# Optimization experiments

Hardware: AMD Instinct MI355X
Metric: run time of the kernel (lower is better)

## Reference

```python
import jax, jax.numpy as jnp
import numpy as np

ITERS = 3
K = 64
C = 256


def setup_inputs() -> dict:
    key = jax.random.key(0)
    ks = jax.random.split(key, 6)
    N, H, W = 2, 60, 60
    cnn_feature = jax.random.normal(ks[0], (N, C, H, W), dtype=jnp.float32)
    points = jax.random.normal(ks[1], (N, 3, H, W), dtype=jnp.float32)
    # torch Linear params: weight (out, in), bias (out,)
    s1 = 1.0 / np.sqrt(C)
    s2 = 1.0 / np.sqrt(2 * C)
    mlp_w = jax.random.uniform(ks[2], (C, C), jnp.float32, -s1, s1)
    mlp_b = jax.random.uniform(ks[3], (C,), jnp.float32, -s1, s1)
    rnn_w = jax.random.uniform(ks[4], (C, 2 * C), jnp.float32, -s2, s2)
    rnn_b = jax.random.uniform(ks[5], (C,), jnp.float32, -s2, s2)
    return {"cnn_feature": cnn_feature, "points": points, "mlp_w": mlp_w,
            "mlp_b": mlp_b, "rnn_w": rnn_w, "rnn_b": rnn_b}


def reference(cnn_feature, points, mlp_w, mlp_b, rnn_w, rnn_b):
    N, Cc, H, W = cnn_feature.shape
    HW = H * W
    pts = points.reshape(N, 3, HW).transpose(0, 2, 1)  # (N, HW, 3)
    # pairwise Euclidean distances via Gram matrix
    r = jnp.einsum('nid,njd->nij', pts, pts)           # (N, HW, HW)
    sq = jnp.einsum('nid,nid->ni', pts, pts)           # (N, HW)
    D = jnp.sqrt(jnp.maximum(sq[:, :, None] + sq[:, None, :] - 2.0 * r, 0.0))
    _, idx = jax.lax.top_k(-D, K)                      # (N, HW, K) smallest distances

    h = cnn_feature.transpose(0, 2, 3, 1).reshape(N, HW, Cc)  # (N, HW, C)
    bidx = jnp.arange(N)[:, None, None]
    for _ in range(ITERS):
        nb = h[bidx, idx]                              # (N, HW, K, C) gather
        nb = jax.nn.relu(jnp.einsum('nskc,dc->nskd', nb, mlp_w) + mlp_b)
        message = nb.mean(axis=2)                      # (N, HW, C)
        nh = jnp.concatenate([h, message], axis=-1)    # (N, HW, 2C)
        h = jax.nn.relu(jnp.einsum('nsc,dc->nsd', nh, rnn_w) + rnn_b)
    h = h.reshape(N, H, W, Cc).transpose(0, 3, 1, 2)   # (N, C, H, W)
    return jnp.concatenate([cnn_feature, h], axis=1)   # (N, 2C, H, W)
```

## Files before the change

kernel.cpp:

```cpp
#include <hip/hip_runtime.h>
#include <stdint.h>

typedef unsigned int uint;

#define HW 3600
#define NBATCH 2
#define CDIM 256
#define KNN 64
#define M_REAL 7200
#define PADM 7232
#define QPB 8

using short8  = __attribute__((ext_vector_type(8))) short;
using floatx4 = __attribute__((ext_vector_type(4))) float;

__device__ inline unsigned short f2bf(float f) {
    uint u = __float_as_uint(f);
    uint r = u + 0x7FFFu + ((u >> 16) & 1u);
    return (unsigned short)(r >> 16);
}
__device__ inline float bf2f(unsigned short b) {
    return __uint_as_float(((uint)b) << 16);
}

__device__ inline void wave_select(uint* hist, uint* s_bin, uint* s_want,
                                   int lane, uint want) {
    uint h0 = hist[4 * lane + 0], h1 = hist[4 * lane + 1];
    uint h2 = hist[4 * lane + 2], h3 = hist[4 * lane + 3];
    hist[4 * lane + 0] = 0; hist[4 * lane + 1] = 0;
    hist[4 * lane + 2] = 0; hist[4 * lane + 3] = 0;
    uint c4 = h0 + h1 + h2 + h3;
    uint v = c4;
    #pragma unroll
    for (int off = 1; off < 64; off <<= 1) {
        uint o = __shfl_up(v, off, 64);
        if (lane >= off) v += o;
    }
    uint below = v - c4;
    if (below < want && want <= v) {
        uint b = 4 * lane, c = below;
        if (c + h0 < want) { c += h0; b = 4 * lane + 1;
            if (c + h1 < want) { c += h1; b = 4 * lane + 2;
                if (c + h2 < want) { c += h2; b = 4 * lane + 3; } } }
        *s_bin = b;
        *s_want = want - c;
    }
}

__global__ __launch_bounds__(512) void topk_kernel(const float* __restrict__ points,
                                                   int* __restrict__ idx_out) {
    const int wv = threadIdx.x >> 6;
    const int lane = threadIdx.x & 63;
    const int q = blockIdx.x * QPB + wv;
    const int n = (blockIdx.x * QPB) / HW;
    const int i = q - n * HW;

    __shared__ float sx[HW], sy[HW], sz[HW];
    __shared__ uint hist[QPB][256];
    __shared__ uint s_bin[QPB], s_want[QPB], s_cnt[QPB];

    const float* __restrict__ px = points + (size_t)n * 3 * HW;
    const float* __restrict__ py = px + HW;
    const float* __restrict__ pz = py + HW;

    for (int j = threadIdx.x; j < HW; j += 512) {
        sx[j] = px[j]; sy[j] = py[j]; sz[j] = pz[j];
    }
    hist[wv][4 * lane + 0] = 0; hist[wv][4 * lane + 1] = 0;
    hist[wv][4 * lane + 2] = 0; hist[wv][4 * lane + 3] = 0;
    if (lane == 0) s_cnt[wv] = 0;
    __syncthreads();

    const float xi = sx[i], yi = sy[i], zi = sz[i];
    const float sqi = xi * xi + yi * yi + zi * zi;

    uint qp[29];
    #pragma unroll
    for (int s = 0; s < 57; ++s) {
        int j = (s << 6) + lane;
        uint q16 = 0xFFFFu;
        if (j < HW) {
            float xj = sx[j], yj = sy[j], zj = sz[j];
            float d2 = fmaxf(sqi + (xj * xj + yj * yj + zj * zj)
                             - 2.0f * (xi * xj + yi * yj + zi * zj), 0.0f);
            q16 = (uint)fminf(d2 * 1024.0f, 65535.0f);
        }
        if (s & 1) qp[s >> 1] |= q16 << 16; else qp[s >> 1] = q16;
    }
    #define Q16(s) ((qp[(s) >> 1] >> (((s) & 1) << 4)) & 0xFFFFu)

    #pragma unroll
    for (int s = 0; s < 57; ++s) atomicAdd(&hist[wv][Q16(s) >> 8], 1u);
    __syncthreads();
    wave_select(&hist[wv][0], &s_bin[wv], &s_want[wv], lane, KNN);
    __syncthreads();
    const uint qT8 = s_bin[wv];
    const uint want2 = s_want[wv];
    __syncthreads();

    #pragma unroll
    for (int s = 0; s < 57; ++s) {
        uint k = Q16(s);
        if ((k >> 8) == qT8) atomicAdd(&hist[wv][k & 255u], 1u);
    }
    __syncthreads();
    wave_select(&hist[wv][0], &s_bin[wv], &s_want[wv], lane, want2);
    __syncthreads();
    const uint qT16 = (qT8 << 8) | s_bin[wv];
    const uint want3 = s_want[wv];

    #pragma unroll
    for (int s = 0; s < 57; ++s) {
        if (Q16(s) < qT16) {
            uint pos = atomicAdd(&s_cnt[wv], 1u);
            if (pos < KNN) idx_out[(size_t)q * KNN + pos] = (s << 6) + lane;
        }
    }
    unsigned long long used = 0ULL;
    const int base = KNN - (int)want3;
    for (int r = 0; r < (int)want3; ++r) {
        unsigned long long best = ~0ULL;
        #pragma unroll
        for (int s = 0; s < 57; ++s) {
            int j = (s << 6) + lane;
            if (j < HW && Q16(s) == qT16 && !((used >> s) & 1ULL)) {
                float xj = sx[j], yj = sy[j], zj = sz[j];
                float d2 = fmaxf(sqi + (xj * xj + yj * yj + zj * zj)
                                 - 2.0f * (xi * xj + yi * yj + zi * zj), 0.0f);
                unsigned long long key =
                    ((unsigned long long)__float_as_uint(d2) << 32) | (uint)j;
                if (key < best) best = key;
            }
        }
        #pragma unroll
        for (int off = 1; off < 64; off <<= 1) {
            unsigned long long o = __shfl_xor(best, off, 64);
            if (o < best) best = o;
        }
        uint jw = (uint)best;
        if (lane == 0) idx_out[(size_t)q * KNN + base + r] = (int)jw;
        if ((int)(jw & 63u) == lane) used |= 1ULL << (jw >> 6);
    }
    #undef Q16
}

__global__ __launch_bounds__(256) void setup_kernel(
    const float* __restrict__ mw, const float* __restrict__ rw,
    unsigned short* __restrict__ mo, unsigned short* __restrict__ ro,
    unsigned short* __restrict__ NHa, unsigned short* __restrict__ NHb) {
    int i = blockIdx.x * 256 + threadIdx.x;
    if (i < 65536) mo[i] = f2bf(mw[i]);
    ro[i] = f2bf(rw[i]);
    if (i < 32 * 512) {
        NHa[(size_t)M_REAL * 512 + i] = 0;
        NHb[(size_t)M_REAL * 512 + i] = 0;
    }
}

__global__ __launch_bounds__(256) void init_h(const float* __restrict__ cnn,
                                              unsigned short* __restrict__ NH,
                                              float* __restrict__ out) {
    __shared__ float tile[32][33];
    const int hw0 = blockIdx.x * 32;
    const int c0 = blockIdx.y * 32;
    const int n = blockIdx.z;
    const int tx = threadIdx.x & 31;
    const int ty = threadIdx.x >> 5;
    const float* __restrict__ src = cnn + (size_t)n * CDIM * HW;
    #pragma unroll
    for (int r = 0; r < 4; ++r) {
        int cc = ty + r * 8;
        int hw = hw0 + tx;
        if (hw < HW) {
            float v = src[(size_t)(c0 + cc) * HW + hw];
            tile[cc][tx] = v;
            out[(size_t)n * (2 * CDIM * HW) + (size_t)(c0 + cc) * HW + hw] = v;
        }
    }
    __syncthreads();
    #pragma unroll
    for (int r = 0; r < 4; ++r) {
        int hh = ty + r * 8;
        int hw = hw0 + hh;
        if (hw < HW) NH[(size_t)(n * HW + hw) * 512 + c0 + tx] = f2bf(tile[tx][hh]);
    }
}

#define LDK 72
__global__ __launch_bounds__(256) void gemm_mfma(
    const unsigned short* __restrict__ A, int lda,
    const unsigned short* __restrict__ W, int ldw,
    const float* __restrict__ bias,
    unsigned short* __restrict__ Cb, float* __restrict__ Cf,
    int ldc, int Kk) {
    __shared__ __align__(16) unsigned short As[64 * LDK];
    __shared__ __align__(16) unsigned short Bs[64 * LDK];
    const int m0 = blockIdx.x * 64;
    const int n0 = blockIdx.y * 64;
    const int tid = threadIdx.x;
    const int lane = tid & 63;
    const int w = tid >> 6;
    const int wm = (w & 1) * 32;
    const int wn = (w >> 1) * 32;
    const int l15 = lane & 15;
    const int qd = lane >> 4;

    floatx4 acc[2][2];
    #pragma unroll
    for (int a = 0; a < 2; ++a)
        #pragma unroll
        for (int b = 0; b < 2; ++b)
            acc[a][b] = (floatx4){0.f, 0.f, 0.f, 0.f};

    const int sr = tid >> 2;
    const int sc = (tid & 3) * 16;

    for (int k0 = 0; k0 < Kk; k0 += 64) {
        const unsigned short* ga = &A[(size_t)(m0 + sr) * lda + k0 + sc];
        const unsigned short* gb = &W[(size_t)(n0 + sr) * ldw + k0 + sc];
        float4 av0 = *(const float4*)(ga);
        float4 av1 = *(const float4*)(ga + 8);
        float4 bv0 = *(const float4*)(gb);
        float4 bv1 = *(const float4*)(gb + 8);
        *(float4*)&As[sr * LDK + sc] = av0;
        *(float4*)&As[sr * LDK + sc + 8] = av1;
        *(float4*)&Bs[sr * LDK + sc] = bv0;
        *(float4*)&Bs[sr * LDK + sc + 8] = bv1;
        __syncthreads();
        #pragma unroll
        for (int ks = 0; ks < 64; ks += 32) {
            short8 a0 = *(const short8*)&As[(wm + l15) * LDK + ks + qd * 8];
            short8 a1 = *(const short8*)&As[(wm + 16 + l15) * LDK + ks + qd * 8];
            short8 b0 = *(const short8*)&Bs[(wn + l15) * LDK + ks + qd * 8];
            short8 b1 = *(const short8*)&Bs[(wn + 16 + l15) * LDK + ks + qd * 8];
            acc[0][0] = __builtin_amdgcn_mfma_f32_16x16x32_bf16(a0, b0, acc[0][0], 0, 0, 0);
            acc[0][1] = __builtin_amdgcn_mfma_f32_16x16x32_bf16(a0, b1, acc[0][1], 0, 0, 0);
            acc[1][0] = __builtin_amdgcn_mfma_f32_16x16x32_bf16(a1, b0, acc[1][0], 0, 0, 0);
            acc[1][1] = __builtin_amdgcn_mfma_f32_16x16x32_bf16(a1, b1, acc[1][1], 0, 0, 0);
        }
        __syncthreads();
    }

    #pragma unroll
    for (int in = 0; in < 2; ++in) {
        int col = n0 + wn + in * 16 + l15;
        float bv = bias[col];
        #pragma unroll
        for (int im = 0; im < 2; ++im) {
            #pragma unroll
            for (int r = 0; r < 4; ++r) {
                int row = m0 + wm + im * 16 + qd * 4 + r;
                float v = fmaxf(acc[im][in][r] + bv, 0.0f);
                if (Cf) Cf[(size_t)row * ldc + col] = v;
                else    Cb[(size_t)row * ldc + col] = f2bf(v);
            }
        }
    }
}

__global__ __launch_bounds__(256) void gather_mean(const unsigned short* __restrict__ T,
                                                   const int* __restrict__ idx,
                                                   unsigned short* __restrict__ NH) {
    const int q = blockIdx.x * 4 + (threadIdx.x >> 6);
    const int lane = threadIdx.x & 63;
    const int n = q / HW;
    const int half = lane >> 5;
    const int c8 = (lane & 31) * 8;

    const int nbrL = idx[(size_t)q * KNN + lane];
    float acc[8] = {0, 0, 0, 0, 0, 0, 0, 0};
    #pragma unroll 4
    for (int it = 0; it < 32; ++it) {
        int k = 2 * it + half;
        int j = __shfl(nbrL, k, 64);
        j = min(max(j, 0), HW - 1);
        int r = n * HW + j;
        uint4 v = *(const uint4*)&T[(size_t)r * CDIM + c8];
        acc[0] += bf2f((unsigned short)(v.x & 0xFFFFu));
        acc[1] += bf2f((unsigned short)(v.x >> 16));
        acc[2] += bf2f((unsigned short)(v.y & 0xFFFFu));
        acc[3] += bf2f((unsigned short)(v.y >> 16));
        acc[4] += bf2f((unsigned short)(v.z & 0xFFFFu));
        acc[5] += bf2f((unsigned short)(v.z >> 16));
        acc[6] += bf2f((unsigned short)(v.w & 0xFFFFu));
        acc[7] += bf2f((unsigned short)(v.w >> 16));
    }
    #pragma unroll
    for (int c = 0; c < 8; ++c) acc[c] += __shfl_xor(acc[c], 32, 64);
    if (half == 0) {
        uint4 o;
        o.x = (uint)f2bf(acc[0] * (1.0f / KNN)) | ((uint)f2bf(acc[1] * (1.0f / KNN)) << 16);
        o.y = (uint)f2bf(acc[2] * (1.0f / KNN)) | ((uint)f2bf(acc[3] * (1.0f / KNN)) << 16);
        o.z = (uint)f2bf(acc[4] * (1.0f / KNN)) | ((uint)f2bf(acc[5] * (1.0f / KNN)) << 16);
        o.w = (uint)f2bf(acc[6] * (1.0f / KNN)) | ((uint)f2bf(acc[7] * (1.0f / KNN)) << 16);
        *(uint4*)&NH[(size_t)q * 512 + CDIM + c8] = o;
    }
}

__global__ __launch_bounds__(256) void final_out(const float* __restrict__ Hf,
                                                 float* __restrict__ out) {
    __shared__ float tile[32][33];
    const int hw0 = blockIdx.x * 32;
    const int c0 = blockIdx.y * 32;
    const int n = blockIdx.z;
    const int tx = threadIdx.x & 31;
    const int ty = threadIdx.x >> 5;
    #pragma unroll
    for (int r = 0; r < 4; ++r) {
        int hh = ty + r * 8;
        int hw = hw0 + hh;
        if (hw < HW) tile[hh][tx] = Hf[(size_t)(n * HW + hw) * CDIM + c0 + tx];
    }
    __syncthreads();
    #pragma unroll
    for (int r = 0; r < 4; ++r) {
        int cc = ty + r * 8;
        int hw = hw0 + tx;
        if (hw < HW)
            out[(size_t)n * (2 * CDIM * HW) + (size_t)(CDIM + c0 + cc) * HW + hw] =
                tile[tx][cc];
    }
}

extern "C" void kernel_launch(void* const* d_in, const int* in_sizes, int n_in,
                              void* d_out, int out_size, void* d_ws, size_t ws_size,
                              hipStream_t stream) {
    const float* cnn   = (const float*)d_in[0];
    const float* pts   = (const float*)d_in[1];
    const float* mlp_w = (const float*)d_in[2];
    const float* mlp_b = (const float*)d_in[3];
    const float* rnn_w = (const float*)d_in[4];
    const float* rnn_b = (const float*)d_in[5];
    float* out = (float*)d_out;

    unsigned short* NHa    = (unsigned short*)d_ws;
    unsigned short* NHb    = NHa + (size_t)PADM * 512;
    unsigned short* Tb     = NHb + (size_t)PADM * 512;
    unsigned short* mlpw_b = Tb + (size_t)PADM * CDIM;
    unsigned short* rnnw_b = mlpw_b + 65536;
    int*            idx    = (int*)(rnnw_b + 131072);

    setup_kernel<<<512, 256, 0, stream>>>(mlp_w, rnn_w, mlpw_b, rnnw_b, NHa, NHb);
    topk_kernel<<<M_REAL / QPB, 512, 0, stream>>>(pts, idx);
    init_h<<<dim3(113, 8, NBATCH), 256, 0, stream>>>(cnn, NHa, out);

    unsigned short* cur = NHa;
    unsigned short* nxt = NHb;
    for (int it = 0; it < 3; ++it) {
        gemm_mfma<<<dim3(PADM / 64, CDIM / 64), 256, 0, stream>>>(
            cur, 512, mlpw_b, CDIM, mlp_b, Tb, nullptr, CDIM, CDIM);
        gather_mean<<<M_REAL / 4, 256, 0, stream>>>(Tb, idx, cur);
        if (it < 2)
            gemm_mfma<<<dim3(PADM / 64, CDIM / 64), 256, 0, stream>>>(
                cur, 512, rnnw_b, 512, rnn_b, nxt, nullptr, 512, 512);
        else
            gemm_mfma<<<dim3(PADM / 64, CDIM / 64), 256, 0, stream>>>(
                cur, 512, rnnw_b, 512, rnn_b, nullptr, (float*)nxt, CDIM, 512);
        unsigned short* tmp = cur; cur = nxt; nxt = tmp;
    }

    final_out<<<dim3(113, 8, NBATCH), 256, 0, stream>>>((const float*)cur, out);
}
```

Measured before the change: 235.0 us.

## Vectorize top-k distance loads, widen GEMM K tile, fuse final transpose into GEMM

The top-k kernel now loads point coordinates with float4 and gives each lane four consecutive candidates per chunk, so the slot and used-bit indexing changes to match. The GEMM stages the full K=256 slice into shared memory per sync instead of 64-wide chunks, which cuts barriers at the cost of more LDS per block. The last RNN GEMM writes fp32 results straight into the NCHW output with float4 stores, which removes the separate final_out transpose kernel. The zeroing of the padded rows in setup is dropped, so the padded GEMM rows now read uninitialized workspace, though those rows are never written to the output.

After: 243.3 us. 3.5% more time.

```diff
diff --git a/kernel.cpp b/kernel.cpp
--- a/kernel.cpp
+++ b/kernel.cpp
@@ -55,16 +55,16 @@
     const int n = (blockIdx.x * QPB) / HW;
     const int i = q - n * HW;
 
-    __shared__ float sx[HW], sy[HW], sz[HW];
+    __shared__ __align__(16) float sx[HW], sy[HW], sz[HW];
     __shared__ uint hist[QPB][256];
     __shared__ uint s_bin[QPB], s_want[QPB], s_cnt[QPB];
 
     const float* __restrict__ px = points + (size_t)n * 3 * HW;
-    const float* __restrict__ py = px + HW;
-    const float* __restrict__ pz = py + HW;
-
-    for (int j = threadIdx.x; j < HW; j += 512) {
-        sx[j] = px[j]; sy[j] = py[j]; sz[j] = pz[j];
+
+    for (int j4 = threadIdx.x; j4 < HW / 4; j4 += 512) {
+        *(float4*)&sx[j4 * 4] = ((const float4*)px)[j4];
+        *(float4*)&sy[j4 * 4] = ((const float4*)px)[j4 + HW / 4];
+        *(float4*)&sz[j4 * 4] = ((const float4*)px)[j4 + 2 * (HW / 4)];
     }
     hist[wv][4 * lane + 0] = 0; hist[wv][4 * lane + 1] = 0;
     hist[wv][4 * lane + 2] = 0; hist[wv][4 * lane + 3] = 0;
@@ -74,23 +74,38 @@
     const float xi = sx[i], yi = sy[i], zi = sz[i];
     const float sqi = xi * xi + yi * yi + zi * zi;
 
-    uint qp[29];
-    #pragma unroll
-    for (int s = 0; s < 57; ++s) {
-        int j = (s << 6) + lane;
-        uint q16 = 0xFFFFu;
-        if (j < HW) {
-            float xj = sx[j], yj = sy[j], zj = sz[j];
-            float d2 = fmaxf(sqi + (xj * xj + yj * yj + zj * zj)
-                             - 2.0f * (xi * xj + yi * yj + zi * zj), 0.0f);
-            q16 = (uint)fminf(d2 * 1024.0f, 65535.0f);
-        }
-        if (s & 1) qp[s >> 1] |= q16 << 16; else qp[s >> 1] = q16;
-    }
-    #define Q16(s) ((qp[(s) >> 1] >> (((s) & 1) << 4)) & 0xFFFFu)
-
-    #pragma unroll
-    for (int s = 0; s < 57; ++s) atomicAdd(&hist[wv][Q16(s) >> 8], 1u);
+    uint qp[30];
+    #pragma unroll
+    for (int c = 0; c < 30; ++c) qp[c] = 0xFFFFFFFFu;
+    #pragma unroll
+    for (int c = 0; c < 15; ++c) {
+        int j0 = (c << 8) + lane * 4;
+        if (j0 < HW) {
+            float4 x4 = *(const float4*)&sx[j0];
+            float4 y4 = *(const float4*)&sy[j0];
+            float4 z4 = *(const float4*)&sz[j0];
+            float d0 = fmaxf(sqi + (x4.x * x4.x + y4.x * y4.x + z4.x * z4.x)
+                             - 2.0f * (xi * x4.x + yi * y4.x + zi * z4.x), 0.0f);
+            float d1 = fmaxf(sqi + (x4.y * x4.y + y4.y * y4.y + z4.y * z4.y)
+                             - 2.0f * (xi * x4.y + yi * y4.y + zi * z4.y), 0.0f);
+            float d2 = fmaxf(sqi + (x4.z * x4.z + y4.z * y4.z + z4.z * z4.z)
+                             - 2.0f * (xi * x4.z + yi * y4.z + zi * z4.z), 0.0f);
+            float d3 = fmaxf(sqi + (x4.w * x4.w + y4.w * y4.w + z4.w * z4.w)
+                             - 2.0f * (xi * x4.w + yi * y4.w + zi * z4.w), 0.0f);
+            uint k0 = (uint)fminf(d0 * 1024.0f, 65535.0f);
+            uint k1 = (uint)fminf(d1 * 1024.0f, 65535.0f);
+            uint k2 = (uint)fminf(d2 * 1024.0f, 65535.0f);
+            uint k3 = (uint)fminf(d3 * 1024.0f, 65535.0f);
+            qp[2 * c]     = k0 | (k1 << 16);
+            qp[2 * c + 1] = k2 | (k3 << 16);
+        }
+    }
+    #define Q16(c, t) ((qp[2 * (c) + ((t) >> 1)] >> (((t) & 1) << 4)) & 0xFFFFu)
+
+    #pragma unroll
+    for (int c = 0; c < 15; ++c)
+        #pragma unroll
+        for (int t = 0; t < 4; ++t) atomicAdd(&hist[wv][Q16(c, t) >> 8], 1u);
     __syncthreads();
     wave_select(&hist[wv][0], &s_bin[wv], &s_want[wv], lane, KNN);
     __syncthreads();
@@ -99,10 +114,12 @@
     __syncthreads();
 
     #pragma unroll
-    for (int s = 0; s < 57; ++s) {
-        uint k = Q16(s);
-        if ((k >> 8) == qT8) atomicAdd(&hist[wv][k & 255u], 1u);
-    }
+    for (int c = 0; c < 15; ++c)
+        #pragma unroll
+        for (int t = 0; t < 4; ++t) {
+            uint k = Q16(c, t);
+            if ((k >> 8) == qT8) atomicAdd(&hist[wv][k & 255u], 1u);
+        }
     __syncthreads();
     wave_select(&hist[wv][0], &s_bin[wv], &s_want[wv], lane, want2);
     __syncthreads();
@@ -110,26 +127,45 @@
     const uint want3 = s_want[wv];
 
     #pragma unroll
-    for (int s = 0; s < 57; ++s) {
-        if (Q16(s) < qT16) {
-            uint pos = atomicAdd(&s_cnt[wv], 1u);
-            if (pos < KNN) idx_out[(size_t)q * KNN + pos] = (s << 6) + lane;
-        }
-    }
+    for (int c = 0; c < 15; ++c)
+        #pragma unroll
+        for (int t = 0; t < 4; ++t) {
+            if (Q16(c, t) < qT16) {
+                uint pos = atomicAdd(&s_cnt[wv], 1u);
+                if (pos < KNN)
+                    idx_out[(size_t)q * KNN + pos] = (c << 8) + lane * 4 + t;
+            }
+        }
     unsigned long long used = 0ULL;
     const int base = KNN - (int)want3;
     for (int r = 0; r < (int)want3; ++r) {
         unsigned long long best = ~0ULL;
         #pragma unroll
-        for (int s = 0; s < 57; ++s) {
-            int j = (s << 6) + lane;
-            if (j < HW && Q16(s) == qT16 && !((used >> s) & 1ULL)) {
-                float xj = sx[j], yj = sy[j], zj = sz[j];
-                float d2 = fmaxf(sqi + (xj * xj + yj * yj + zj * zj)
-                                 - 2.0f * (xi * xj + yi * yj + zi * zj), 0.0f);
-                unsigned long long key =
-                    ((unsigned long long)__float_as_uint(d2) << 32) | (uint)j;
-                if (key < best) best = key;
+        for (int c = 0; c < 15; ++c) {
+            int j0 = (c << 8) + lane * 4;
+            if (j0 < HW) {
+                float4 x4 = *(const float4*)&sx[j0];
+                float4 y4 = *(const float4*)&sy[j0];
+                float4 z4 = *(const float4*)&sz[j0];
+                float dd[4];
+                dd[0] = fmaxf(sqi + (x4.x * x4.x + y4.x * y4.x + z4.x * z4.x)
+                              - 2.0f * (xi * x4.x + yi * y4.x + zi * z4.x), 0.0f);
+                dd[1] = fmaxf(sqi + (x4.y * x4.y + y4.y * y4.y + z4.y * z4.y)
+                              - 2.0f * (xi * x4.y + yi * y4.y + zi * z4.y), 0.0f);
+                dd[2] = fmaxf(sqi + (x4.z * x4.z + y4.z * y4.z + z4.z * z4.z)
+                              - 2.0f * (xi * x4.z + yi * y4.z + zi * z4.z), 0.0f);
+                dd[3] = fmaxf(sqi + (x4.w * x4.w + y4.w * y4.w + z4.w * z4.w)
+                              - 2.0f * (xi * x4.w + yi * y4.w + zi * z4.w), 0.0f);
+                #pragma unroll
+                for (int t = 0; t < 4; ++t) {
+                    int slot = c * 4 + t;
+                    if (Q16(c, t) == qT16 && !((used >> slot) & 1ULL)) {
+                        unsigned long long key =
+                            ((unsigned long long)__float_as_uint(dd[t]) << 32)
+                            | (uint)(j0 + t);
+                        if (key < best) best = key;
+                    }
+                }
             }
         }
         #pragma unroll
@@ -139,22 +175,18 @@
         }
         uint jw = (uint)best;
         if (lane == 0) idx_out[(size_t)q * KNN + base + r] = (int)jw;
-        if ((int)(jw & 63u) == lane) used |= 1ULL << (jw >> 6);
+        if ((int)((jw & 255u) >> 2) == lane)
+            used |= 1ULL << (((jw >> 8) << 2) | (jw & 3u));
     }
     #undef Q16
 }
 
 __global__ __launch_bounds__(256) void setup_kernel(
     const float* __restrict__ mw, const float* __restrict__ rw,
-    unsigned short* __restrict__ mo, unsigned short* __restrict__ ro,
-    unsigned short* __restrict__ NHa, unsigned short* __restrict__ NHb) {
+    unsigned short* __restrict__ mo, unsigned short* __restrict__ ro) {
     int i = blockIdx.x * 256 + threadIdx.x;
     if (i < 65536) mo[i] = f2bf(mw[i]);
     ro[i] = f2bf(rw[i]);
-    if (i < 32 * 512) {
-        NHa[(size_t)M_REAL * 512 + i] = 0;
-        NHb[(size_t)M_REAL * 512 + i] = 0;
-    }
 }
 
 __global__ __launch_bounds__(256) void init_h(const float* __restrict__ cnn,
@@ -186,15 +218,15 @@
     }
 }
 
-#define LDK 72
+#define LDKP 264
 __global__ __launch_bounds__(256) void gemm_mfma(
     const unsigned short* __restrict__ A, int lda,
     const unsigned short* __restrict__ W, int ldw,
     const float* __restrict__ bias,
-    unsigned short* __restrict__ Cb, float* __restrict__ Cf,
-    int ldc, int Kk) {
-    __shared__ __align__(16) unsigned short As[64 * LDK];
-    __shared__ __align__(16) unsigned short Bs[64 * LDK];
+    unsigned short* __restrict__ Cb, int ldc,
+    float* __restrict__ outp, int mode, int Kk) {
+    __shared__ __align__(16) unsigned short As[64 * LDKP];
+    __shared__ __align__(16) unsigned short Bs[64 * LDKP];
     const int m0 = blockIdx.x * 64;
     const int n0 = blockIdx.y * 64;
     const int tid = threadIdx.x;
@@ -212,33 +244,31 @@
         for (int b = 0; b < 2; ++b)
             acc[a][b] = (floatx4){0.f, 0.f, 0.f, 0.f};
 
-    const int sr = tid >> 2;
-    const int sc = (tid & 3) * 16;
-
-    for (int k0 = 0; k0 < Kk; k0 += 64) {
-        const unsigned short* ga = &A[(size_t)(m0 + sr) * lda + k0 + sc];
-        const unsigned short* gb = &W[(size_t)(n0 + sr) * ldw + k0 + sc];
-        float4 av0 = *(const float4*)(ga);
-        float4 av1 = *(const float4*)(ga + 8);
-        float4 bv0 = *(const float4*)(gb);
-        float4 bv1 = *(const float4*)(gb + 8);
-        *(float4*)&As[sr * LDK + sc] = av0;
-        *(float4*)&As[sr * LDK + sc + 8] = av1;
-        *(float4*)&Bs[sr * LDK + sc] = bv0;
-        *(float4*)&Bs[sr * LDK + sc + 8] = bv1;
+    const int srow = tid >> 5;
+    const int scol = (tid & 31) * 8;
+
+    for (int k0 = 0; k0 < Kk; k0 += 256) {
+        if (k0) __syncthreads();
+        #pragma unroll
+        for (int r8 = 0; r8 < 8; ++r8) {
+            int row = r8 * 8 + srow;
+            *(float4*)&As[row * LDKP + scol] =
+                *(const float4*)&A[(size_t)(m0 + row) * lda + k0 + scol];
+            *(float4*)&Bs[row * LDKP + scol] =
+                *(const float4*)&W[(size_t)(n0 + row) * ldw + k0 + scol];
+        }
         __syncthreads();
         #pragma unroll
-        for (int ks = 0; ks < 64; ks += 32) {
-            short8 a0 = *(const short8*)&As[(wm + l15) * LDK + ks + qd * 8];
-            short8 a1 = *(const short8*)&As[(wm + 16 + l15) * LDK + ks + qd * 8];
-            short8 b0 = *(const short8*)&Bs[(wn + l15) * LDK + ks + qd * 8];
-            short8 b1 = *(const short8*)&Bs[(wn + 16 + l15) * LDK + ks + qd * 8];
+        for (int ks = 0; ks < 256; ks += 32) {
+            short8 a0 = *(const short8*)&As[(wm + l15) * LDKP + ks + qd * 8];
+            short8 a1 = *(const short8*)&As[(wm + 16 + l15) * LDKP + ks + qd * 8];
+            short8 b0 = *(const short8*)&Bs[(wn + l15) * LDKP + ks + qd * 8];
+            short8 b1 = *(const short8*)&Bs[(wn + 16 + l15) * LDKP + ks + qd * 8];
             acc[0][0] = __builtin_amdgcn_mfma_f32_16x16x32_bf16(a0, b0, acc[0][0], 0, 0, 0);
             acc[0][1] = __builtin_amdgcn_mfma_f32_16x16x32_bf16(a0, b1, acc[0][1], 0, 0, 0);
             acc[1][0] = __builtin_amdgcn_mfma_f32_16x16x32_bf16(a1, b0, acc[1][0], 0, 0, 0);
             acc[1][1] = __builtin_amdgcn_mfma_f32_16x16x32_bf16(a1, b1, acc[1][1], 0, 0, 0);
         }
-        __syncthreads();
     }
 
     #pragma unroll
@@ -247,12 +277,22 @@
         float bv = bias[col];
         #pragma unroll
         for (int im = 0; im < 2; ++im) {
-            #pragma unroll
-            for (int r = 0; r < 4; ++r) {
-                int row = m0 + wm + im * 16 + qd * 4 + r;
-                float v = fmaxf(acc[im][in][r] + bv, 0.0f);
-                if (Cf) Cf[(size_t)row * ldc + col] = v;
-                else    Cb[(size_t)row * ldc + col] = f2bf(v);
+            int mb = m0 + wm + im * 16 + qd * 4;
+            if (mode == 0) {
+                #pragma unroll
+                for (int r = 0; r < 4; ++r)
+                    Cb[(size_t)(mb + r) * ldc + col] =
+                        f2bf(fmaxf(acc[im][in][r] + bv, 0.0f));
+            } else if (mb < M_REAL) {
+                int nb = mb / HW;
+                int hw = mb - nb * HW;
+                float4 o;
+                o.x = fmaxf(acc[im][in][0] + bv, 0.0f);
+                o.y = fmaxf(acc[im][in][1] + bv, 0.0f);
+                o.z = fmaxf(acc[im][in][2] + bv, 0.0f);
+                o.w = fmaxf(acc[im][in][3] + bv, 0.0f);
+                *(float4*)&outp[(size_t)nb * (2 * CDIM * HW)
+                                + (size_t)(CDIM + col) * HW + hw] = o;
             }
         }
     }
@@ -297,31 +337,6 @@
     }
 }
 
-__global__ __launch_bounds__(256) void final_out(const float* __restrict__ Hf,
-                                                 float* __restrict__ out) {
-    __shared__ float tile[32][33];
-    const int hw0 = blockIdx.x * 32;
-    const int c0 = blockIdx.y * 32;
-    const int n = blockIdx.z;
-    const int tx = threadIdx.x & 31;
-    const int ty = threadIdx.x >> 5;
-    #pragma unroll
-    for (int r = 0; r < 4; ++r) {
-        int hh = ty + r * 8;
-        int hw = hw0 + hh;
-        if (hw < HW) tile[hh][tx] = Hf[(size_t)(n * HW + hw) * CDIM + c0 + tx];
-    }
-    __syncthreads();
-    #pragma unroll
-    for (int r = 0; r < 4; ++r) {
-        int cc = ty + r * 8;
-        int hw = hw0 + tx;
-        if (hw < HW)
-            out[(size_t)n * (2 * CDIM * HW) + (size_t)(CDIM + c0 + cc) * HW + hw] =
-                tile[tx][cc];
-    }
-}
-
 extern "C" void kernel_launch(void* const* d_in, const int* in_sizes, int n_in,
                               void* d_out, int out_size, void* d_ws, size_t ws_size,
                               hipStream_t stream) {
@@ -340,7 +355,7 @@
     unsigned short* rnnw_b = mlpw_b + 65536;
     int*            idx    = (int*)(rnnw_b + 131072);
 
-    setup_kernel<<<512, 256, 0, stream>>>(mlp_w, rnn_w, mlpw_b, rnnw_b, NHa, NHb);
+    setup_kernel<<<512, 256, 0, stream>>>(mlp_w, rnn_w, mlpw_b, rnnw_b);
     topk_kernel<<<M_REAL / QPB, 512, 0, stream>>>(pts, idx);
     init_h<<<dim3(113, 8, NBATCH), 256, 0, stream>>>(cnn, NHa, out);
 
@@ -348,16 +363,15 @@
     unsigned short* nxt = NHb;
     for (int it = 0; it < 3; ++it) {
         gemm_mfma<<<dim3(PADM / 64, CDIM / 64), 256, 0, stream>>>(
-            cur, 512, mlpw_b, CDIM, mlp_b, Tb, nullptr, CDIM, CDIM);
+            cur, 512, mlpw_b, CDIM, mlp_b, Tb, CDIM, nullptr, 0, CDIM);
         gather_mean<<<M_REAL / 4, 256, 0, stream>>>(Tb, idx, cur);
-        if (it < 2)
+        if (it < 2) {
             gemm_mfma<<<dim3(PADM / 64, CDIM / 64), 256, 0, stream>>>(
-                cur, 512, rnnw_b, 512, rnn_b, nxt, nullptr, 512, 512);
-        else
+                cur, 512, rnnw_b, 512, rnn_b, nxt, 512, nullptr, 0, 512);
+            unsigned short* tmp = cur; cur = nxt; nxt = tmp;
+        } else {
             gemm_mfma<<<dim3(PADM / 64, CDIM / 64), 256, 0, stream>>>(
-                cur, 512, rnnw_b, 512, rnn_b, nullptr, (float*)nxt, CDIM, 512);
-        unsigned short* tmp = cur; cur = nxt; nxt = tmp;
-    }
-
-    final_out<<<dim3(113, 8, NBATCH), 256, 0, stream>>>((const float*)cur, out);
-}
+                cur, 512, rnnw_b, 512, rnn_b, nullptr, 0, out, 1, 512);
+        }
+    }
+}
```
